# Kernel optimization log

Measured on AMD Instinct MI355X. Metric: run time of the kernel, lower is better.

Reference implementation:

```python
import jax, jax.numpy as jnp
import numpy as np

N = 50000      # num nodes
E = 800000     # num edges (before self loops)
F_IN = 128     # fea_size
D = 128        # g_dim_per_layer[i]
H = 4          # heads
C = D // H     # out_channels per head
NEG_SLOPE = 0.2  # PyG GATConv default leaky_relu slope


def setup_inputs() -> dict:
    key = jax.random.key(0)
    ks = jax.random.split(key, 20)
    inp = {
        "x": jax.random.normal(ks[0], (N, F_IN), dtype=jnp.float32),
        "edge_index": jax.random.randint(ks[1], (2, E), 0, N, dtype=jnp.int32),
        "w0": jax.random.normal(ks[2], (F_IN, D), dtype=jnp.float32) * 0.05,
        "b0": jnp.zeros((D,), dtype=jnp.float32),
    }
    for i in (1, 2, 3):
        k = 4 * i
        inp[f"w{i}"] = jax.random.normal(ks[k], (D, D), dtype=jnp.float32) * 0.05
        inp[f"a_src{i}"] = jax.random.normal(ks[k + 1], (H, C), dtype=jnp.float32) * 0.1
        inp[f"a_dst{i}"] = jax.random.normal(ks[k + 2], (H, C), dtype=jnp.float32) * 0.1
        inp[f"b{i}"] = jnp.zeros((D,), dtype=jnp.float32)
    return inp


def _gat_layer(x, src, dst, w, a_src, a_dst, b):
    # PyG GATConv (eval mode, dropout inactive, add_self_loops already applied)
    n = x.shape[0]
    xp = (x @ w).reshape(n, H, C)                       # [N,H,C]
    al_s = jnp.einsum("nhc,hc->nh", xp, a_src)          # [N,H]
    al_d = jnp.einsum("nhc,hc->nh", xp, a_dst)          # [N,H]
    e = jax.nn.leaky_relu(al_s[src] + al_d[dst], NEG_SLOPE)  # [E',H]
    # softmax over incoming edges of each destination node
    m = jax.ops.segment_max(e, dst, num_segments=n)
    e = jnp.exp(e - m[dst])
    s = jax.ops.segment_sum(e, dst, num_segments=n)
    alpha = e / s[dst]                                  # [E',H]
    msg = alpha[:, :, None] * xp[src]                   # [E',H,C]
    out = jax.ops.segment_sum(msg, dst, num_segments=n)  # [N,H,C]
    return out.reshape(n, H * C) + b


def reference(x, edge_index, w0, b0, w1, a_src1, a_dst1, b1,
              w2, a_src2, a_dst2, b2, w3, a_src3, a_dst3, b3):
    n = x.shape[0]
    loops = jnp.arange(n, dtype=edge_index.dtype)
    ei = jnp.concatenate([edge_index, jnp.stack([loops, loops])], axis=1)
    src, dst = ei[0], ei[1]  # messages flow src -> dst (PyG convention)

    h = x @ w0 + b0
    h = jax.nn.relu(h + _gat_layer(h, src, dst, w1, a_src1, a_dst1, b1))
    h = jax.nn.relu(h + _gat_layer(h, src, dst, w2, a_src2, a_dst2, b2))
    return _gat_layer(h, src, dst, w3, a_src3, a_dst3, b3)
```

## Files before the change

### kernel.cpp

```cpp
#include <hip/hip_runtime.h>

#define F 128
#define HEADS 4
#define NEG 0.2f
#define CAP 40
#define CAPP 44
#define CB 6144
#define HTS 136

typedef unsigned short u16;
typedef unsigned int u32;
typedef __attribute__((ext_vector_type(8))) unsigned short us8;
typedef __attribute__((ext_vector_type(8))) short short8;
typedef __attribute__((ext_vector_type(4))) float f32x4;

__device__ __forceinline__ float bf2f(u16 u) {
  union { u32 i; float f; } v; v.i = ((u32)u) << 16; return v.f;
}
__device__ __forceinline__ float bflo(u32 p) {
  union { u32 i; float f; } v; v.i = p << 16; return v.f;
}
__device__ __forceinline__ float bfhi(u32 p) {
  union { u32 i; float f; } v; v.i = p & 0xFFFF0000u; return v.f;
}
__device__ __forceinline__ u16 f2bf(float f) {
  union { u32 i; float f; } v; v.f = f;
  if (((v.i >> 23) & 0xFF) == 0xFF) return 0;
  u32 r = v.i + 0x7FFF + ((v.i >> 16) & 1);
  return (u16)(r >> 16);
}
__device__ __forceinline__ float sane(float f) {
  union { u32 i; float f; } v; v.f = f;
  return (((v.i >> 23) & 0xFF) == 0xFF) ? 0.f : f;
}
__device__ __forceinline__ u16 bfsane(u16 u) {
  return (((u >> 7) & 0xFF) == 0xFF) ? (u16)0 : u;
}

__device__ __forceinline__ bool detect_f32_wave(const u16* __restrict__ p) {
  int lane = threadIdx.x & 63;
  const us8* q = (const us8*)p + lane * 4;
  int c = 0;
  #pragma unroll
  for (int k = 0; k < 4; k++) {
    us8 v = q[k];
    #pragma unroll
    for (int j = 0; j < 8; j++) { unsigned e = (v[j] >> 7) & 0xFF; c += (e >= 0xF8); }
  }
  #pragma unroll
  for (int off = 32; off; off >>= 1) c += __shfl_xor(c, off);
  return c > 4;
}

__global__ __launch_bounds__(256) void fill_const_bf16(u16* __restrict__ p, u16 v, int n) {
  int i = blockIdx.x * blockDim.x + threadIdx.x;
  if (i < n) p[i] = v;
}

__global__ __launch_bounds__(256) void setup(
    const void* w0, const void* w1, const void* w2, const void* w3,
    const void* b0, const void* b1, const void* b2, const void* b3,
    const void* as1, const void* ad1, const void* as2, const void* ad2,
    const void* as3, const void* ad3,
    u16* __restrict__ wsz, u16* __restrict__ avf, float* __restrict__ par,
    int* __restrict__ flg, int* __restrict__ gcur) {
  __shared__ float vv[8][128];
  bool f32 = detect_f32_wave((const u16*)w0);
  int blk = blockIdx.x, tid = threadIdx.x;
  if (blk < 32) {
    int idx = blk * 256 + tid;
    int layer = idx >> 11;
    int rest  = idx & 2047;
    int lane = rest & 63;
    int ts   = rest >> 6;
    int s = ts & 3, t = ts >> 2;
    int kbase = s * 32 + (lane >> 4) * 8;
    int nn    = t * 16 + (lane & 15);
    const void* W = (layer == 0) ? w0 : (layer == 1) ? w1 : (layer == 2) ? w2 : w3;
    us8 o;
    #pragma unroll
    for (int j = 0; j < 8; j++) {
      int off = (kbase + j) * F + nn;
      o[j] = f32 ? f2bf(sane(((const float*)W)[off])) : bfsane(((const u16*)W)[off]);
    }
    *(us8*)(wsz + (size_t)idx * 8) = o;
  } else if (blk < 37) {
    int t = (blk - 32) * 256 + tid;
    if (t < 1280) {
      const void* tab[10] = {b0, b1, b2, b3, as1, ad1, as2, ad2, as3, ad3};
      const void* src = tab[t >> 7];
      int idx = t & 127;
      float v = f32 ? ((const float*)src)[idx] : bf2f(((const u16*)src)[idx]);
      par[t] = sane(v);
    }
  } else if (blk == 37) {
    gcur[tid] = 0;
    if (tid == 0) flg[0] = f32 ? 1 : 0;
  } else {
    int l = blk - 38;
    const void* W   = (l == 0) ? w1 : (l == 1) ? w2 : w3;
    const void* asp = (l == 0) ? as1 : (l == 1) ? as2 : as3;
    const void* adp = (l == 0) ? ad1 : (l == 1) ? ad2 : ad3;
    for (int e = tid; e < 1024; e += 256) {
      int vec = e >> 7, k = e & 127;
      int h = vec & 3;
      const void* av = (vec < 4) ? asp : adp;
      float sum = 0.f;
      for (int c = 0; c < 32; c++) {
        int col = h * 32 + c;
        float wv_ = f32 ? ((const float*)W)[k * F + col] : bf2f(((const u16*)W)[k * F + col]);
        float aa  = f32 ? ((const float*)av)[col]        : bf2f(((const u16*)av)[col]);
        sum += sane(wv_) * sane(aa);
      }
      vv[vec][k] = sane(sum);
    }
    __syncthreads();
    int s = tid >> 6, lane = tid & 63;
    int quad = lane >> 4, l15 = lane & 15;
    int kbase = s * 32 + quad * 8;
    us8 o;
    #pragma unroll
    for (int j = 0; j < 8; j++)
      o[j] = (l15 < 8) ? f2bf(vv[l15][kbase + j]) : (u16)0;
    *(us8*)(avf + (((size_t)l * 4 + s) * 64 + lane) * 8) = o;
  }
}

__device__ __forceinline__ void gemm_tile(
    int m0, int lane, const void* __restrict__ A, int f32in,
    const u16* __restrict__ wszL, const float* __restrict__ biasc,
    const u16* __restrict__ avfL, u16* __restrict__ Cm,
    float* __restrict__ al_s, float* __restrict__ al_d, int nrows) {
  int quad = lane >> 4, l15 = lane & 15;
  int mrow = m0 + l15;
  int ml = mrow < nrows ? mrow : (nrows - 1);
  short8 af[4];
  if (f32in) {
    const float* ar = (const float*)A + (size_t)ml * F;
    #pragma unroll
    for (int s = 0; s < 4; s++) {
      float4 u = *(const float4*)(ar + s * 32 + quad * 8);
      float4 v = *(const float4*)(ar + s * 32 + quad * 8 + 4);
      short8 p;
      p[0] = (short)f2bf(sane(u.x)); p[1] = (short)f2bf(sane(u.y));
      p[2] = (short)f2bf(sane(u.z)); p[3] = (short)f2bf(sane(u.w));
      p[4] = (short)f2bf(sane(v.x)); p[5] = (short)f2bf(sane(v.y));
      p[6] = (short)f2bf(sane(v.z)); p[7] = (short)f2bf(sane(v.w));
      af[s] = p;
    }
  } else {
    const u16* ar = (const u16*)A + (size_t)ml * F;
    #pragma unroll
    for (int s = 0; s < 4; s++) af[s] = *(const short8*)(ar + s * 32 + quad * 8);
  }

  f32x4 acc[8];
  #pragma unroll
  for (int t = 0; t < 8; t++) acc[t] = (f32x4){0.f, 0.f, 0.f, 0.f};
  f32x4 accL = (f32x4){0.f, 0.f, 0.f, 0.f};

  #pragma unroll
  for (int s = 0; s < 4; s++) {
    short8 bfr[8];
    #pragma unroll
    for (int t = 0; t < 8; t++)
      bfr[t] = *(const short8*)(wszL + (size_t)(((t << 2) | s) * 64 + lane) * 8);
    if (avfL) {
      short8 av = *(const short8*)(avfL + (size_t)(s * 64 + lane) * 8);
      accL = __builtin_amdgcn_mfma_f32_16x16x32_bf16(af[s], av, accL, 0, 0, 0);
    }
    #pragma unroll
    for (int t = 0; t < 8; t++)
      acc[t] = __builtin_amdgcn_mfma_f32_16x16x32_bf16(af[s], bfr[t], acc[t], 0, 0, 0);
  }

  #pragma unroll
  for (int t = 0; t < 8; t++) {
    int cc = t * 16 + l15;
    float b = biasc ? biasc[cc] : 0.f;
    #pragma unroll
    for (int r = 0; r < 4; r++) {
      int row = m0 + quad * 4 + r;
      if (row < nrows) Cm[(size_t)row * F + cc] = f2bf(sane(acc[t][r] + b));
    }
  }
  if (avfL && l15 < 8) {
    float* dst = (l15 < 4) ? al_s : al_d;
    int h = l15 & 3;
    #pragma unroll
    for (int r = 0; r < 4; r++) {
      int row = m0 + quad * 4 + r;
      if (row < nrows) dst[(size_t)row * 4 + h] = sane(accL[r]);
    }
  }
}

__device__ __forceinline__ void scatter_body(const int* __restrict__ ei,
                                             int* __restrict__ gcur,
                                             int2* __restrict__ ebuf,
                                             int E, int E2, int n, int blk) {
  __shared__ int lcnt[256];
  __shared__ int gbase[256];
  int tid = threadIdx.x;
  lcnt[tid] = 0;
  __syncthreads();
  int srcv[16], dstv[16], rnk[16];
  #pragma unroll
  for (int i = 0; i < 16; i++) {
    int e = blk * 4096 + i * 256 + tid;
    rnk[i] = -1;
    if (e < E2) {
      int src, dst;
      if (e < E) { src = ei[e]; dst = ei[E + e]; }
      else       { src = dst = e - E; }
      if ((unsigned)dst < (unsigned)n) {
        srcv[i] = src; dstv[i] = dst;
        rnk[i] = atomicAdd(&lcnt[dst >> 8], 1);
      }
    }
  }
  __syncthreads();
  int c = lcnt[tid];
  gbase[tid] = c ? atomicAdd(&gcur[tid], c) : 0;
  __syncthreads();
  #pragma unroll
  for (int i = 0; i < 16; i++) {
    if (rnk[i] >= 0) {
      int b = dstv[i] >> 8;
      int slot = gbase[b] + rnk[i];
      if (slot < CB) ebuf[(size_t)b * CB + slot] = make_int2(srcv[i], dstv[i]);
    }
  }
}

__device__ __forceinline__ void fill_body(const int* __restrict__ gcur,
                                          const int2* __restrict__ ebuf,
                                          int* __restrict__ rp,
                                          int* __restrict__ col, int n, int b) {
  __shared__ int sc[256];
  __shared__ int ncnt[256];
  __shared__ int nofs[256];
  __shared__ int wsums[4];
  __shared__ int total_s;
  int tid = threadIdx.x, lane = tid & 63, wv = tid >> 6;
  int v = min(gcur[tid], CB);
  int x = v;
  #pragma unroll
  for (int off = 1; off < 64; off <<= 1) {
    int t = __shfl_up(x, off);
    if (lane >= off) x += t;
  }
  if (lane == 63) wsums[wv] = x;
  __syncthreads();
  int add = 0;
  for (int w = 0; w < wv; w++) add += wsums[w];
  sc[tid] = add + x - v;
  if (tid == 255) total_s = add + x;
  __syncthreads();
  int tot = min(gcur[b], CB);
  int colbase = sc[b];
  const int2* eb = ebuf + (size_t)b * CB;
  ncnt[tid] = 0;
  __syncthreads();
  for (int j = tid; j < tot; j += 256) atomicAdd(&ncnt[eb[j].y & 255], 1);
  __syncthreads();
  v = ncnt[tid];
  x = v;
  #pragma unroll
  for (int off = 1; off < 64; off <<= 1) {
    int t = __shfl_up(x, off);
    if (lane >= off) x += t;
  }
  if (lane == 63) wsums[wv] = x;
  __syncthreads();
  add = 0;
  for (int w = 0; w < wv; w++) add += wsums[w];
  nofs[tid] = add + x - v;
  int node = (b << 8) + tid;
  if (node < n) rp[node] = colbase + nofs[tid];
  if (b == 0 && tid == 0) rp[n] = total_s;
  __syncthreads();
  ncnt[tid] = 0;
  __syncthreads();
  for (int j = tid; j < tot; j += 256) {
    int2 e = eb[j];
    int ln = e.y & 255;
    int r = atomicAdd(&ncnt[ln], 1);
    col[colbase + nofs[ln] + r] = e.x;
  }
}

__global__ __launch_bounds__(256) void scatter_gemm0(
    const int* __restrict__ ei, int* __restrict__ gcur, int2* __restrict__ ebuf,
    int E, int E2, int n, int SB,
    const void* __restrict__ x, const int* __restrict__ flg,
    const u16* __restrict__ wsz, const float* __restrict__ b0c,
    u16* __restrict__ hio) {
  int blk = blockIdx.x;
  if (blk < SB) {
    scatter_body(ei, gcur, ebuf, E, E2, n, blk);
  } else {
    int tid = threadIdx.x, wv = tid >> 6, lane = tid & 63;
    int m0 = (blk - SB) * 64 + wv * 16;
    gemm_tile(m0, lane, x, flg[0], wsz, b0c, nullptr, hio, nullptr, nullptr, n);
  }
}

__global__ __launch_bounds__(256) void fill_gemm1(
    const int* __restrict__ gcur, const int2* __restrict__ ebuf,
    int* __restrict__ rp, int* __restrict__ col, int n, int NBv,
    const void* __restrict__ hA, const u16* __restrict__ wszL,
    const u16* __restrict__ avfL, u16* __restrict__ xp,
    float* __restrict__ al_s, float* __restrict__ al_d) {
  int blk = blockIdx.x;
  if (blk < NBv) {
    fill_body(gcur, ebuf, rp, col, n, blk);
  } else {
    int tid = threadIdx.x, wv = tid >> 6, lane = tid & 63;
    int m0 = (blk - NBv) * 64 + wv * 16;
    gemm_tile(m0, lane, hA, 0, wszL, nullptr, avfL, xp, al_s, al_d, n);
  }
}

#define ACC8(w_, P_)                                    \
  a0 += (w_) * bflo((P_).x); a1 += (w_) * bfhi((P_).x); \
  a2 += (w_) * bflo((P_).y); a3 += (w_) * bfhi((P_).y); \
  a4 += (w_) * bflo((P_).z); a5 += (w_) * bfhi((P_).z); \
  a6 += (w_) * bflo((P_).w); a7 += (w_) * bfhi((P_).w);

__global__ __launch_bounds__(256, 8) void gat_agg_gemm(
    const u16* __restrict__ xp, const float* __restrict__ al_s,
    const float* __restrict__ al_d, const int* __restrict__ row_ptr,
    const int* __restrict__ col, const float* __restrict__ biasc,
    u16* __restrict__ hio, const int* __restrict__ flgp,
    int n, int E2, int mode,
    const u16* __restrict__ wszL, const u16* __restrict__ avfL,
    u16* __restrict__ xpo, float* __restrict__ also_, float* __restrict__ aldo) {
  __shared__ int   sb[4][4][CAP];
  __shared__ float wb[4][4][4][CAPP];
  __shared__ u16   ht[16 * HTS];
  int tid = threadIdx.x;
  int wv = tid >> 6, lane = tid & 63;
  int q = lane >> 4, g = lane & 15;
  int node = blockIdx.x * 16 + wv * 4 + q;
  bool active = node < n;
  int beg = 0, end = 0;
  float ald_[4] = {0.f, 0.f, 0.f, 0.f};
  if (active) {
    beg = row_ptr[node]; end = row_ptr[node + 1];
    if (beg < 0) beg = 0; if (beg > E2) beg = E2;
    if (end < beg) end = beg; if (end > E2) end = E2;
    float4 qd = ((const float4*)al_d)[node];
    ald_[0] = qd.x; ald_[1] = qd.y; ald_[2] = qd.z; ald_[3] = qd.w;
  }
  int deg = end - beg;
  int ch = g * 8, head = g >> 2;
  u32 cb = (u32)g * 16;
  const char* xpb = (const char*)xp;
  float a0 = 0.f, a1 = 0.f, a2 = 0.f, a3 = 0.f;
  float a4 = 0.f, a5 = 0.f, a6 = 0.f, a7 = 0.f;
  float inv;

  if (deg <= CAP) {
    float er[3][4];
    float m4[4] = {-1e30f, -1e30f, -1e30f, -1e30f};
    #pragma unroll
    for (int it = 0; it < 3; it++) {
      int jj = g + it * 16;
      if (jj < deg) {
        int src = col[beg + jj];
        if ((unsigned)src >= (unsigned)n) src = node;
        sb[wv][q][jj] = src;
        float4 qs = ((const float4*)al_s)[src];
        float as_[4] = {qs.x, qs.y, qs.z, qs.w};
        #pragma unroll
        for (int h = 0; h < 4; h++) {
          float e = as_[h] + ald_[h];
          e = (e > 0.f) ? e : NEG * e;
          er[it][h] = e;
          m4[h] = fmaxf(m4[h], e);
        }
      }
    }
    #pragma unroll
    for (int off = 8; off; off >>= 1)
      #pragma unroll
      for (int h = 0; h < 4; h++) m4[h] = fmaxf(m4[h], __shfl_xor(m4[h], off));
    float s4[4] = {0.f, 0.f, 0.f, 0.f};
    #pragma unroll
    for (int it = 0; it < 3; it++) {
      int jj = g + it * 16;
      if (jj < deg) {
        #pragma unroll
        for (int h = 0; h < 4; h++) {
          float w = __expf(er[it][h] - m4[h]);
          s4[h] += w;
          wb[wv][q][h][jj] = w;
        }
      }
    }
    #pragma unroll
    for (int off = 8; off; off >>= 1)
      #pragma unroll
      for (int h = 0; h < 4; h++) s4[h] += __shfl_xor(s4[h], off);
    inv = (s4[head] > 0.f) ? 1.f / s4[head] : 0.f;
    __asm__ volatile("s_waitcnt lgkmcnt(0)" ::: "memory");
    const int* srow = sb[wv][q];
    const float* wrow = wb[wv][q][head];
    int j = 0;
    if (deg >= 4) {
      int4 sa = *(const int4*)(srow);
      float4 wa = *(const float4*)(wrow);
      uint4 P0 = *(const uint4*)(xpb + (((u32)sa.x << 8) + cb));
      uint4 P1 = *(const uint4*)(xpb + (((u32)sa.y << 8) + cb));
      uint4 P2 = *(const uint4*)(xpb + (((u32)sa.z << 8) + cb));
      uint4 P3 = *(const uint4*)(xpb + (((u32)sa.w << 8) + cb));
      for (; j + 8 <= deg; j += 4) {
        int4 sn = *(const int4*)(srow + j + 4);
        float4 wn = *(const float4*)(wrow + j + 4);
        uint4 Q0 = *(const uint4*)(xpb + (((u32)sn.x << 8) + cb));
        uint4 Q1 = *(const uint4*)(xpb + (((u32)sn.y << 8) + cb));
        uint4 Q2 = *(const uint4*)(xpb + (((u32)sn.z << 8) + cb));
        uint4 Q3 = *(const uint4*)(xpb + (((u32)sn.w << 8) + cb));
        ACC8(wa.x, P0); ACC8(wa.y, P1); ACC8(wa.z, P2); ACC8(wa.w, P3);
        wa = wn; P0 = Q0; P1 = Q1; P2 = Q2; P3 = Q3;
      }
      ACC8(wa.x, P0); ACC8(wa.y, P1); ACC8(wa.z, P2); ACC8(wa.w, P3);
      j += 4;
    }
    for (; j < deg; j++) {
      int s0 = srow[j];
      float w0 = wrow[j];
      uint4 p0 = *(const uint4*)(xpb + (((u32)s0 << 8) + cb));
      ACC8(w0, p0);
    }
    a0 *= inv; a1 *= inv; a2 *= inv; a3 *= inv;
    a4 *= inv; a5 *= inv; a6 *= inv; a7 *= inv;
  } else {
    float m = -1.0e30f, s = 0.f;
    for (int j = beg; j < end; ++j) {
      int src = col[j];
      if ((unsigned)src >= (unsigned)n) continue;
      float e = al_s[src * 4 + head] + ald_[head];
      e = (e > 0.f) ? e : NEG * e;
      float mn = fmaxf(m, e);
      float scale = __expf(m - mn);
      float w = __expf(e - mn);
      uint4 pv = *(const uint4*)(xpb + (((u32)src << 8) + cb));
      s = s * scale + w;
      a0 = a0 * scale + w * bflo(pv.x); a1 = a1 * scale + w * bfhi(pv.x);
      a2 = a2 * scale + w * bflo(pv.y); a3 = a3 * scale + w * bfhi(pv.y);
      a4 = a4 * scale + w * bflo(pv.z); a5 = a5 * scale + w * bfhi(pv.z);
      a6 = a6 * scale + w * bflo(pv.w); a7 = a7 * scale + w * bfhi(pv.w);
      m = mn;
    }
    inv = (s > 0.f) ? 1.f / s : 0.f;
    a0 *= inv; a1 *= inv; a2 *= inv; a3 *= inv;
    a4 *= inv; a5 *= inv; a6 *= inv; a7 *= inv;
  }

  if (mode == 0) {
    uint4 st = make_uint4(0u, 0u, 0u, 0u);
    if (active) {
      float4 b4a = *(const float4*)(biasc + ch);
      float4 b4b = *(const float4*)(biasc + ch + 4);
      float o0 = sane(a0) + b4a.x, o1 = sane(a1) + b4a.y;
      float o2 = sane(a2) + b4a.z, o3 = sane(a3) + b4a.w;
      float o4 = sane(a4) + b4b.x, o5 = sane(a5) + b4b.y;
      float o6 = sane(a6) + b4b.z, o7 = sane(a7) + b4b.w;
      size_t o = (size_t)node * F + ch;
      uint4 hv = *(const uint4*)(hio + o);
      o0 = fmaxf(bflo(hv.x) + o0, 0.f);
      o1 = fmaxf(bfhi(hv.x) + o1, 0.f);
      o2 = fmaxf(bflo(hv.y) + o2, 0.f);
      o3 = fmaxf(bfhi(hv.y) + o3, 0.f);
      o4 = fmaxf(bflo(hv.z) + o4, 0.f);
      o5 = fmaxf(bfhi(hv.z) + o5, 0.f);
      o6 = fmaxf(bflo(hv.w) + o6, 0.f);
      o7 = fmaxf(bfhi(hv.w) + o7, 0.f);
      st.x = ((u32)f2bf(sane(o1)) << 16) | (u32)f2bf(sane(o0));
      st.y = ((u32)f2bf(sane(o3)) << 16) | (u32)f2bf(sane(o2));
      st.z = ((u32)f2bf(sane(o5)) << 16) | (u32)f2bf(sane(o4));
      st.w = ((u32)f2bf(sane(o7)) << 16) | (u32)f2bf(sane(o6));
      *(uint4*)(hio + o) = st;
    }
    *(uint4*)&ht[(wv * 4 + q) * HTS + ch] = st;
    __syncthreads();

    int quad = lane >> 4, l15 = lane & 15;
    short8 af[4];
    #pragma unroll
    for (int s = 0; s < 4; s++)
      af[s] = *(const short8*)&ht[l15 * HTS + s * 32 + quad * 8];
    f32x4 acc0 = (f32x4){0.f, 0.f, 0.f, 0.f};
    f32x4 acc1 = (f32x4){0.f, 0.f, 0.f, 0.f};
    f32x4 accL = (f32x4){0.f, 0.f, 0.f, 0.f};
    int t0 = wv * 2;
    #pragma unroll
    for (int s = 0; s < 4; s++) {
      short8 bv0 = *(const short8*)(wszL + (size_t)(((t0 << 2) | s) * 64 + lane) * 8);
      short8 bv1 = *(const short8*)(wszL + (size_t)((((t0 + 1) << 2) | s) * 64 + lane) * 8);
      if (wv == 0) {
        short8 av = *(const short8*)(avfL + (size_t)(s * 64 + lane) * 8);
        accL = __builtin_amdgcn_mfma_f32_16x16x32_bf16(af[s], av, accL, 0, 0, 0);
      }
      acc0 = __builtin_amdgcn_mfma_f32_16x16x32_bf16(af[s], bv0, acc0, 0, 0, 0);
      acc1 = __builtin_amdgcn_mfma_f32_16x16x32_bf16(af[s], bv1, acc1, 0, 0, 0);
    }
    int row0 = blockIdx.x * 16;
    #pragma unroll
    for (int tt = 0; tt < 2; tt++) {
      f32x4 ac = tt ? acc1 : acc0;
      int cc = (t0 + tt) * 16 + l15;
      #pragma unroll
      for (int r = 0; r < 4; r++) {
        int row = row0 + quad * 4 + r;
        if (row < n) xpo[(size_t)row * F + cc] = f2bf(sane(ac[r]));
      }
    }
    if (wv == 0 && l15 < 8) {
      float* dst = (l15 < 4) ? also_ : aldo;
      int h = l15 & 3;
      #pragma unroll
      for (int r = 0; r < 4; r++) {
        int row = row0 + quad * 4 + r;
        if (row < n) dst[(size_t)row * 4 + h] = sane(accL[r]);
      }
    }
  } else {
    if (!active) return;
    float4 b4a = *(const float4*)(biasc + ch);
    float4 b4b = *(const float4*)(biasc + ch + 4);
    float o0 = sane(a0) + b4a.x, o1 = sane(a1) + b4a.y;
    float o2 = sane(a2) + b4a.z, o3 = sane(a3) + b4a.w;
    float o4 = sane(a4) + b4b.x, o5 = sane(a5) + b4b.y;
    float o6 = sane(a6) + b4b.z, o7 = sane(a7) + b4b.w;
    size_t o = (size_t)node * F + ch;
    if (flgp[0]) {
      float4 s1 = {sane(o0), sane(o1), sane(o2), sane(o3)};
      float4 s2 = {sane(o4), sane(o5), sane(o6), sane(o7)};
      *(float4*)((float*)hio + o) = s1;
      *(float4*)((float*)hio + o + 4) = s2;
    } else {
      uint4 st;
      st.x = ((u32)f2bf(sane(o1)) << 16) | (u32)f2bf(sane(o0));
      st.y = ((u32)f2bf(sane(o3)) << 16) | (u32)f2bf(sane(o2));
      st.z = ((u32)f2bf(sane(o5)) << 16) | (u32)f2bf(sane(o4));
      st.w = ((u32)f2bf(sane(o7)) << 16) | (u32)f2bf(sane(o6));
      *(uint4*)(hio + o) = st;
    }
  }
}

extern "C" void kernel_launch(void* const* d_in, const int* in_sizes, int n_in,
                              void* d_out, int out_size, void* d_ws, size_t ws_size,
                              hipStream_t stream) {
  const int* ei = (const int*)d_in[1];

  const int N  = in_sizes[0] / F;
  const int E  = in_sizes[1] / 2;
  const int E2 = E + N;
  const int NB = (N + 255) >> 8;
  const int SB = (E2 + 4095) / 4096;
  const int GB64  = (N + 63) / 64;
  const int AGGB  = (N + 15) / 16;

  uintptr_t base = ((uintptr_t)d_ws + 255) & ~(uintptr_t)255;
  size_t off_par = 0;
  size_t off_flg = off_par + (size_t)1536 * 4;
  size_t off_wsz = off_flg + 256;
  size_t off_avf = off_wsz + (size_t)65536 * 2;
  size_t off_xp  = off_avf + (size_t)6144 * 2;
  size_t off_als = off_xp  + (size_t)N * F * 2;
  size_t off_ald = off_als + (size_t)N * HEADS * 4;
  size_t off_gc  = off_ald + (size_t)N * HEADS * 4;
  size_t off_rp  = off_gc  + 1024;
  size_t off_col = off_rp  + (size_t)(N + 1) * 4;
  size_t off_eb  = (off_col + (size_t)E2 * 4 + 255) & ~(size_t)255;
  size_t off_xp2 = (off_eb + (size_t)NB * CB * 8 + 255) & ~(size_t)255;
  size_t off_als2 = off_xp2 + (size_t)N * F * 2;
  size_t off_ald2 = off_als2 + (size_t)N * HEADS * 4;
  size_t need    = off_ald2 + (size_t)N * HEADS * 4 + 512 + ((uintptr_t)d_ws & 255);

  if (ws_size < need) {
    fill_const_bf16<<<(out_size + 255) / 256, 256, 0, stream>>>(
        (u16*)d_out, (u16)0x4316, out_size);
    return;
  }

  float* par   = (float*)(base + off_par);
  int* flg     = (int*)(base + off_flg);
  u16* wsz     = (u16*)(base + off_wsz);
  u16* avf     = (u16*)(base + off_avf);
  u16* xpA     = (u16*)(base + off_xp);
  float* alsA  = (float*)(base + off_als);
  float* aldA  = (float*)(base + off_ald);
  int* gcur    = (int*)(base + off_gc);
  int* row_ptr = (int*)(base + off_rp);
  int* col     = (int*)(base + off_col);
  int2* ebuf   = (int2*)(base + off_eb);
  u16* xpB     = (u16*)(base + off_xp2);
  float* alsB  = (float*)(base + off_als2);
  float* aldB  = (float*)(base + off_ald2);

  float* bc[4];
  for (int l = 0; l < 4; ++l) bc[l] = par + (size_t)l * 128;

  u16* hio = (u16*)d_out;

  setup<<<41, 256, 0, stream>>>(
      d_in[2], d_in[4], d_in[8], d_in[12],
      d_in[3], d_in[7], d_in[11], d_in[15],
      d_in[5], d_in[6], d_in[9], d_in[10], d_in[13], d_in[14],
      wsz, avf, par, flg, gcur);

  scatter_gemm0<<<SB + GB64, 256, 0, stream>>>(
      ei, gcur, ebuf, E, E2, N, SB, d_in[0], flg, wsz, bc[0], hio);

  fill_gemm1<<<NB + GB64, 256, 0, stream>>>(
      gcur, ebuf, row_ptr, col, N, NB,
      hio, wsz + (size_t)1 * 16384, avf, xpA, alsA, aldA);

  gat_agg_gemm<<<AGGB, 256, 0, stream>>>(
      xpA, alsA, aldA, row_ptr, col, bc[1], hio, flg, N, E2, 0,
      wsz + (size_t)2 * 16384, avf + (size_t)1 * 2048, xpB, alsB, aldB);

  gat_agg_gemm<<<AGGB, 256, 0, stream>>>(
      xpB, alsB, aldB, row_ptr, col, bc[2], hio, flg, N, E2, 0,
      wsz + (size_t)3 * 16384, avf + (size_t)2 * 2048, xpA, alsA, aldA);

  gat_agg_gemm<<<AGGB, 256, 0, stream>>>(
      xpA, alsA, aldA, row_ptr, col, bc[3], hio, flg, N, E2, 1,
      nullptr, nullptr, nullptr, nullptr, nullptr);
}
```

Baseline: 274.5 us.

## Reorder aggregation nodes by in-degree class for balanced warp work

Computes a per-node degree class during CSR fill, builds a permutation that groups nodes of similar in-degree with a counting sort in a new kernel, and has the aggregation kernels process nodes in that order. Quarter-warps handling nodes in the same wave then see similar edge counts, which reduces divergence and tail imbalance in the edge loops. Output rows and fused GEMM results are written back through the permutation. The cost is an extra kernel launch, extra workspace, and scattered rather than contiguous row access to node data and outputs.

Result: slower. 416.5 us (+51.8%).

```diff
diff --git a/kernel.cpp b/kernel.cpp
--- a/kernel.cpp
+++ b/kernel.cpp
@@ -7,6 +7,7 @@
 #define CAPP 44
 #define CB 6144
 #define HTS 136
+#define DCLS 128
 
 typedef unsigned short u16;
 typedef unsigned int u32;
@@ -63,7 +64,7 @@
     const void* as1, const void* ad1, const void* as2, const void* ad2,
     const void* as3, const void* ad3,
     u16* __restrict__ wsz, u16* __restrict__ avf, float* __restrict__ par,
-    int* __restrict__ flg, int* __restrict__ gcur) {
+    int* __restrict__ flg, int* __restrict__ gcur, int* __restrict__ dcnt) {
   __shared__ float vv[8][128];
   bool f32 = detect_f32_wave((const u16*)w0);
   int blk = blockIdx.x, tid = threadIdx.x;
@@ -95,6 +96,7 @@
     }
   } else if (blk == 37) {
     gcur[tid] = 0;
+    if (tid < DCLS) dcnt[tid] = 0;
     if (tid == 0) flg[0] = f32 ? 1 : 0;
   } else {
     int l = blk - 38;
@@ -236,7 +238,9 @@
 __device__ __forceinline__ void fill_body(const int* __restrict__ gcur,
                                           const int2* __restrict__ ebuf,
                                           int* __restrict__ rp,
-                                          int* __restrict__ col, int n, int b) {
+                                          int* __restrict__ col, int n, int b,
+                                          int* __restrict__ rnkb,
+                                          int* __restrict__ dcnt) {
   __shared__ int sc[256];
   __shared__ int ncnt[256];
   __shared__ int nofs[256];
@@ -277,7 +281,11 @@
   for (int w = 0; w < wv; w++) add += wsums[w];
   nofs[tid] = add + x - v;
   int node = (b << 8) + tid;
-  if (node < n) rp[node] = colbase + nofs[tid];
+  if (node < n) {
+    rp[node] = colbase + nofs[tid];
+    int dc = v < (DCLS - 1) ? v : (DCLS - 1);
+    rnkb[node] = atomicAdd(&dcnt[dc], 1);
+  }
   if (b == 0 && tid == 0) rp[n] = total_s;
   __syncthreads();
   ncnt[tid] = 0;
@@ -311,14 +319,42 @@
     int* __restrict__ rp, int* __restrict__ col, int n, int NBv,
     const void* __restrict__ hA, const u16* __restrict__ wszL,
     const u16* __restrict__ avfL, u16* __restrict__ xp,
-    float* __restrict__ al_s, float* __restrict__ al_d) {
+    float* __restrict__ al_s, float* __restrict__ al_d,
+    int* __restrict__ rnkb, int* __restrict__ dcnt) {
   int blk = blockIdx.x;
   if (blk < NBv) {
-    fill_body(gcur, ebuf, rp, col, n, blk);
+    fill_body(gcur, ebuf, rp, col, n, blk, rnkb, dcnt);
   } else {
     int tid = threadIdx.x, wv = tid >> 6, lane = tid & 63;
     int m0 = (blk - NBv) * 64 + wv * 16;
     gemm_tile(m0, lane, hA, 0, wszL, nullptr, avfL, xp, al_s, al_d, n);
+  }
+}
+
+__global__ __launch_bounds__(256) void mkperm(
+    const int* __restrict__ rp, const int* __restrict__ rnkb,
+    const int* __restrict__ dcnt, int* __restrict__ perm, int n) {
+  __shared__ int sbase[DCLS];
+  int tid = threadIdx.x, lane = tid & 63;
+  if (tid < 64) {
+    int c0 = dcnt[lane], c1 = dcnt[64 + lane];
+    int x0 = c0, x1 = c1;
+    #pragma unroll
+    for (int off = 1; off < 64; off <<= 1) {
+      int t0 = __shfl_up(x0, off);
+      int t1 = __shfl_up(x1, off);
+      if (lane >= off) { x0 += t0; x1 += t1; }
+    }
+    int tot0 = __shfl(x0, 63);
+    sbase[lane] = x0 - c0;
+    sbase[64 + lane] = tot0 + x1 - c1;
+  }
+  __syncthreads();
+  int node = blockIdx.x * 256 + tid;
+  if (node < n) {
+    int deg = rp[node + 1] - rp[node];
+    int dc = deg < (DCLS - 1) ? deg : (DCLS - 1);
+    perm[sbase[dc] + rnkb[node]] = node;
   }
 }
 
@@ -333,17 +369,20 @@
     const float* __restrict__ al_d, const int* __restrict__ row_ptr,
     const int* __restrict__ col, const float* __restrict__ biasc,
     u16* __restrict__ hio, const int* __restrict__ flgp,
-    int n, int E2, int mode,
+    int n, int E2, int mode, const int* __restrict__ perm,
     const u16* __restrict__ wszL, const u16* __restrict__ avfL,
     u16* __restrict__ xpo, float* __restrict__ also_, float* __restrict__ aldo) {
   __shared__ int   sb[4][4][CAP];
   __shared__ float wb[4][4][4][CAPP];
   __shared__ u16   ht[16 * HTS];
+  __shared__ int   pnid[16];
   int tid = threadIdx.x;
   int wv = tid >> 6, lane = tid & 63;
   int q = lane >> 4, g = lane & 15;
-  int node = blockIdx.x * 16 + wv * 4 + q;
-  bool active = node < n;
+  int gid = blockIdx.x * 16 + wv * 4 + q;
+  bool active = gid < n;
+  int node = active ? perm[gid] : 0;
+  if (active && g == 0) pnid[wv * 4 + q] = node;
   int beg = 0, end = 0;
   float ald_[4] = {0.f, 0.f, 0.f, 0.f};
   if (active) {
@@ -514,8 +553,8 @@
       int cc = (t0 + tt) * 16 + l15;
       #pragma unroll
       for (int r = 0; r < 4; r++) {
-        int row = row0 + quad * 4 + r;
-        if (row < n) xpo[(size_t)row * F + cc] = f2bf(sane(ac[r]));
+        int slot = quad * 4 + r;
+        if (row0 + slot < n) xpo[(size_t)pnid[slot] * F + cc] = f2bf(sane(ac[r]));
       }
     }
     if (wv == 0 && l15 < 8) {
@@ -523,8 +562,8 @@
       int h = l15 & 3;
       #pragma unroll
       for (int r = 0; r < 4; r++) {
-        int row = row0 + quad * 4 + r;
-        if (row < n) dst[(size_t)row * 4 + h] = sane(accL[r]);
+        int slot = quad * 4 + r;
+        if (row0 + slot < n) dst[(size_t)pnid[slot] * 4 + h] = sane(accL[r]);
       }
     }
   } else {
@@ -574,7 +613,10 @@
   size_t off_als = off_xp  + (size_t)N * F * 2;
   size_t off_ald = off_als + (size_t)N * HEADS * 4;
   size_t off_gc  = off_ald + (size_t)N * HEADS * 4;
-  size_t off_rp  = off_gc  + 1024;
+  size_t off_dc  = off_gc  + 1024;
+  size_t off_rk  = off_dc  + (size_t)DCLS * 4;
+  size_t off_pm  = off_rk  + (size_t)N * 4;
+  size_t off_rp  = off_pm  + (size_t)N * 4;
   size_t off_col = off_rp  + (size_t)(N + 1) * 4;
   size_t off_eb  = (off_col + (size_t)E2 * 4 + 255) & ~(size_t)255;
   size_t off_xp2 = (off_eb + (size_t)NB * CB * 8 + 255) & ~(size_t)255;
@@ -596,6 +638,9 @@
   float* alsA  = (float*)(base + off_als);
   float* aldA  = (float*)(base + off_ald);
   int* gcur    = (int*)(base + off_gc);
+  int* dcnt    = (int*)(base + off_dc);
+  int* rnkb    = (int*)(base + off_rk);
+  int* perm    = (int*)(base + off_pm);
   int* row_ptr = (int*)(base + off_rp);
   int* col     = (int*)(base + off_col);
   int2* ebuf   = (int2*)(base + off_eb);
@@ -612,24 +657,26 @@
       d_in[2], d_in[4], d_in[8], d_in[12],
       d_in[3], d_in[7], d_in[11], d_in[15],
       d_in[5], d_in[6], d_in[9], d_in[10], d_in[13], d_in[14],
-      wsz, avf, par, flg, gcur);
+      wsz, avf, par, flg, gcur, dcnt);
 
   scatter_gemm0<<<SB + GB64, 256, 0, stream>>>(
       ei, gcur, ebuf, E, E2, N, SB, d_in[0], flg, wsz, bc[0], hio);
 
   fill_gemm1<<<NB + GB64, 256, 0, stream>>>(
       gcur, ebuf, row_ptr, col, N, NB,
-      hio, wsz + (size_t)1 * 16384, avf, xpA, alsA, aldA);
+      hio, wsz + (size_t)1 * 16384, avf, xpA, alsA, aldA, rnkb, dcnt);
+
+  mkperm<<<NB, 256, 0, stream>>>(row_ptr, rnkb, dcnt, perm, N);
 
   gat_agg_gemm<<<AGGB, 256, 0, stream>>>(
-      xpA, alsA, aldA, row_ptr, col, bc[1], hio, flg, N, E2, 0,
+      xpA, alsA, aldA, row_ptr, col, bc[1], hio, flg, N, E2, 0, perm,
       wsz + (size_t)2 * 16384, avf + (size_t)1 * 2048, xpB, alsB, aldB);
 
   gat_agg_gemm<<<AGGB, 256, 0, stream>>>(
-      xpB, alsB, aldB, row_ptr, col, bc[2], hio, flg, N, E2, 0,
+      xpB, alsB, aldB, row_ptr, col, bc[2], hio, flg, N, E2, 0, perm,
       wsz + (size_t)3 * 16384, avf + (size_t)2 * 2048, xpA, alsA, aldA);
 
   gat_agg_gemm<<<AGGB, 256, 0, stream>>>(
-      xpA, alsA, aldA, row_ptr, col, bc[3], hio, flg, N, E2, 1,
+      xpA, alsA, aldA, row_ptr, col, bc[3], hio, flg, N, E2, 1, perm,
       nullptr, nullptr, nullptr, nullptr, nullptr);
 }
```
